# Optimization experiments

Hardware: AMD Instinct MI355X
Metric: run time of the kernel (lower is better)

## Reference

```python
import jax, jax.numpy as jnp
from jax import lax
import numpy as np


def _conv3x3(x, w, b):
    # x: [B,C,H,W], w: [O,I,3,3] (OIHW), SAME padding, stride 1
    y = lax.conv_general_dilated(x, w, window_strides=(1, 1), padding='SAME',
                                 dimension_numbers=('NCHW', 'OIHW', 'NCHW'))
    return y + b[None, :, None, None]


def setup_inputs() -> dict:
    key = jax.random.key(0)
    ks = jax.random.split(key, 9)
    B, C, H, W = 4, 64, 64, 64
    wscale = 1.0 / np.sqrt(C * 9)  # keep conv outputs / attention logits sane
    x = jax.random.normal(ks[0], (B, C, H, W), dtype=jnp.float32)
    wq = jax.random.normal(ks[1], (C, C, 3, 3), dtype=jnp.float32) * wscale
    bq = jax.random.normal(ks[2], (C,), dtype=jnp.float32) * 0.1
    wk = jax.random.normal(ks[3], (C, C, 3, 3), dtype=jnp.float32) * wscale
    bk = jax.random.normal(ks[4], (C,), dtype=jnp.float32) * 0.1
    wv = jax.random.normal(ks[5], (C, C, 3, 3), dtype=jnp.float32) * wscale
    bv = jax.random.normal(ks[6], (C,), dtype=jnp.float32) * 0.1
    pos_gamma = jax.random.normal(ks[7], (1,), dtype=jnp.float32)
    chan_gamma = jax.random.normal(ks[8], (1,), dtype=jnp.float32)
    return {'x': x, 'wq': wq, 'bq': bq, 'wk': wk, 'bk': bk, 'wv': wv, 'bv': bv,
            'pos_gamma': pos_gamma, 'chan_gamma': chan_gamma}


def reference(x, wq, bq, wk, bk, wv, bv, pos_gamma, chan_gamma):
    B, C, H, W = x.shape
    N = H * W
    # position (spatial) self-attention over N = H*W locations
    q = _conv3x3(x, wq, bq).reshape(B, C, N)
    k = _conv3x3(x, wk, bk).reshape(B, C, N)
    v = _conv3x3(x, wv, bv).reshape(B, C, N)
    # attn[b,i,j] = softmax_j( sum_c q[b,c,i] * k[b,c,j] )
    pos_attn = jax.nn.softmax(jnp.einsum('bci,bcj->bij', q, k), axis=-1)
    # pos_out[b,c,j] = sum_i v[b,c,i] * attn[b,i,j]  (matches torch.bmm(v, attn))
    pos = jnp.einsum('bci,bij->bcj', v, pos_attn).reshape(B, C, H, W)
    pos_out = pos_gamma * pos + x
    # channel self-attention over C channels (x is its own q/k/v)
    xf = x.reshape(B, C, N)
    chan_attn = jax.nn.softmax(jnp.einsum('bcn,bdn->bcd', xf, xf), axis=-1)
    chan = jnp.einsum('bcd,bdn->bcn', chan_attn, xf).reshape(B, C, H, W)
    chan_out = chan_gamma * chan + x
    return pos_out + chan_out
```

## Files before the change

### kernel.cpp

```cpp
#include <hip/hip_runtime.h>

#define OFF_POS   0u
#define OFF_Q2    1048576u
#define OFF_K2    2097152u
#define OFF_V2    3145728u
#define OFF_VLO   3670016u
#define OFF_WT    4194304u
#define OFF_INVL  4452352u
#define OFF_GPART 4468736u
#define OFF_A     4730880u
#define WS_FLOATS 4747264u

typedef short s8v __attribute__((ext_vector_type(8)));
typedef float f4v __attribute__((ext_vector_type(4)));
typedef float f16v __attribute__((ext_vector_type(16)));

#define MFMA32(a, b, c) __builtin_amdgcn_mfma_f32_32x32x16_bf16((a), (b), (c), 0, 0, 0)

__device__ __forceinline__ unsigned short bf16_rne(float f) {
    union { float f; unsigned int u; } v; v.f = f;
    unsigned int r = v.u + 0x7FFFu + ((v.u >> 16) & 1u);
    return (unsigned short)(r >> 16);
}
__device__ __forceinline__ float bf2f(unsigned short h) {
    union { unsigned int u; float f; } t; t.u = ((unsigned int)h) << 16;
    return t.f;
}
__device__ __forceinline__ void split2(float f, unsigned short& h, unsigned short& l) {
    unsigned short hh = bf16_rne(f);
    h = hh;
    l = bf16_rne(f - bf2f(hh));
}
__device__ __forceinline__ unsigned int pk2(float lo, float hi) {
    return (unsigned int)bf16_rne(lo) | ((unsigned int)bf16_rne(hi) << 16);
}
__device__ __forceinline__ void pl32swap(unsigned int& a, unsigned int& b) {
    asm volatile("v_permlane32_swap_b32 %0, %1" : "+v"(a), "+v"(b));
}
__device__ __forceinline__ s8v mk8(unsigned int w0, unsigned int w1,
                                   unsigned int w2, unsigned int w3) {
    union { unsigned int u[4]; s8v v; } t;
    t.u[0] = w0; t.u[1] = w1; t.u[2] = w2; t.u[3] = w3;
    return t.v;
}
__device__ __forceinline__ f16v zero16() {
    f16v z;
#pragma unroll
    for (int i = 0; i < 16; ++i) z[i] = 0.0f;
    return z;
}


__global__ void k_wtrans(const float* __restrict__ wq, const float* __restrict__ wk,
                         const float* __restrict__ wv, unsigned short* __restrict__ wf) {
    int t = blockIdx.x * 256 + threadIdx.x;
    int f = t >> 9, pos = t & 511;
    int lane = pos >> 3, e = pos & 7;
    int oc = f & 1, kst = (f >> 1) & 3;
    int ct = f >> 3;
    int tap = ct % 9, conv = ct / 9;
    int o = oc * 32 + (lane & 31);
    int ci = kst * 16 + (lane >> 5) * 8 + e;
    const float* w = (conv == 0) ? wq : (conv == 1) ? wk : wv;
    float v = w[(o * 64 + ci) * 9 + tap];
    unsigned short hh, ll;
    split2(v, hh, ll);
    wf[(f * 2 + 0) * 512 + pos] = hh;
    wf[(f * 2 + 1) * 512 + pos] = ll;
}

__global__ __launch_bounds__(384) void k_conv(
        const float* __restrict__ x, const unsigned short* __restrict__ wf,
        const float* __restrict__ bq, const float* __restrict__ bk, const float* __restrict__ bv,
        unsigned short* __restrict__ Q2, unsigned short* __restrict__ K2,
        unsigned short* __restrict__ V2, unsigned short* __restrict__ VLO) {
    int nb = blockIdx.x;
    int b = blockIdx.y;
    int h = nb >> 1, w0 = (nb & 1) * 32;

    __shared__ unsigned short xwh[6528];
    __shared__ unsigned short xwl[6528];

    int tid = threadIdx.x;
    for (int idx = tid; idx < 6528; idx += 384) {
        int W = idx % 34;
        int c = (idx / 34) & 63;
        int dy = idx / (34 * 64);
        int hs = h + dy - 1, wi = w0 + W - 1;
        float v = 0.0f;
        if (hs >= 0 && hs < 64 && wi >= 0 && wi < 64)
            v = x[((b * 64 + c) * 64 + hs) * 64 + wi];
        unsigned short hh_, ll_;
        split2(v, hh_, ll_);
        int row = dy * 34 + W;
        int byt = row * 128 + c * 2;
        int swz = byt ^ ((row & 7) << 4);
        *(unsigned short*)((char*)xwh + swz) = hh_;
        *(unsigned short*)((char*)xwl + swz) = ll_;
    }
    __syncthreads();

    int lane = tid & 63, wv = tid >> 6;
    int conv = wv >> 1, oc = wv & 1;
    int hh = lane >> 5, l31 = lane & 31;

    const float* bias = (conv == 0) ? bq : (conv == 1) ? bk : bv;
    f16v D;
    if (conv < 2) {
#pragma unroll
        for (int r = 0; r < 16; ++r)
            D[r] = bias[oc * 32 + (r & 3) + 8 * (r >> 2) + 4 * hh];
    } else {
        float bvv = bias[oc * 32 + l31];
#pragma unroll
        for (int r = 0; r < 16; ++r) D[r] = bvv;
    }

#pragma unroll
    for (int tap = 0; tap < 9; ++tap) {
        int dy = tap / 3, dx = tap % 3;
#pragma unroll
        for (int kst = 0; kst < 4; ++kst) {
            int f = ((conv * 9 + tap) * 4 + kst) * 2 + oc;
            s8v Wh = *(const s8v*)(wf + (f * 2 + 0) * 512 + lane * 8);
            s8v Wl = *(const s8v*)(wf + (f * 2 + 1) * 512 + lane * 8);
            int row = dy * 34 + dx + l31;
            int byt = row * 128 + kst * 32 + hh * 16;
            int swz = byt ^ ((row & 7) << 4);
            s8v Xh = *(const s8v*)((const char*)xwh + swz);
            s8v Xl = *(const s8v*)((const char*)xwl + swz);
            if (conv < 2) {
                D = MFMA32(Wh, Xh, D);
                D = MFMA32(Wh, Xl, D);
                D = MFMA32(Wl, Xh, D);
            } else {
                D = MFMA32(Xh, Wh, D);
                D = MFMA32(Xl, Wh, D);
                D = MFMA32(Xh, Wl, D);
            }
        }
    }

    unsigned short sh[16], sl[16];
#pragma unroll
    for (int r = 0; r < 16; ++r) split2(D[r], sh[r], sl[r]);
    unsigned int ah0 = sh[0] | ((unsigned int)sh[1] << 16), ah1 = sh[2] | ((unsigned int)sh[3] << 16);
    unsigned int ah2 = sh[4] | ((unsigned int)sh[5] << 16), ah3 = sh[6] | ((unsigned int)sh[7] << 16);
    pl32swap(ah0, ah2); pl32swap(ah1, ah3);
    s8v F0h = mk8(ah0, ah1, ah2, ah3);
    unsigned int al0 = sl[0] | ((unsigned int)sl[1] << 16), al1 = sl[2] | ((unsigned int)sl[3] << 16);
    unsigned int al2 = sl[4] | ((unsigned int)sl[5] << 16), al3 = sl[6] | ((unsigned int)sl[7] << 16);
    pl32swap(al0, al2); pl32swap(al1, al3);
    s8v F0l = mk8(al0, al1, al2, al3);
    unsigned int bh0 = sh[8] | ((unsigned int)sh[9] << 16), bh1 = sh[10] | ((unsigned int)sh[11] << 16);
    unsigned int bh2 = sh[12] | ((unsigned int)sh[13] << 16), bh3 = sh[14] | ((unsigned int)sh[15] << 16);
    pl32swap(bh0, bh2); pl32swap(bh1, bh3);
    s8v F1h = mk8(bh0, bh1, bh2, bh3);
    unsigned int bl0 = sl[8] | ((unsigned int)sl[9] << 16), bl1 = sl[10] | ((unsigned int)sl[11] << 16);
    unsigned int bl2 = sl[12] | ((unsigned int)sl[13] << 16), bl3 = sl[14] | ((unsigned int)sl[15] << 16);
    pl32swap(bl0, bl2); pl32swap(bl1, bl3);
    s8v F1l = mk8(bl0, bl1, bl2, bl3);

    if (conv < 2) {
        unsigned short* dst = (conv == 0) ? Q2 : K2;
        size_t b0 = (size_t)(((b * 128 + nb) * 4 + oc * 2 + 0) * 2) * 512 + lane * 8;
        size_t b1 = (size_t)(((b * 128 + nb) * 4 + oc * 2 + 1) * 2) * 512 + lane * 8;
        *(s8v*)(dst + b0) = F0h;
        *(s8v*)(dst + b0 + 512) = F0l;
        *(s8v*)(dst + b1) = F1h;
        *(s8v*)(dst + b1 + 512) = F1l;
    } else {
        size_t b0 = (size_t)((((b * 128 + nb) * 2 + 0) * 2 + oc)) * 512 + lane * 8;
        size_t b1 = (size_t)((((b * 128 + nb) * 2 + 1) * 2 + oc)) * 512 + lane * 8;
        *(s8v*)(V2 + b0) = F0h;
        *(s8v*)(VLO + b0) = F0l;
        *(s8v*)(V2 + b1) = F1h;
        *(s8v*)(VLO + b1) = F1l;
    }
}

__global__ __launch_bounds__(256) void k_gram(const float* __restrict__ x, float* __restrict__ Gp64) {
    int nc = blockIdx.x, b = blockIdx.y;
    __shared__ float xs[64 * 65];
    int tid = threadIdx.x;
#pragma unroll
    for (int it = 0; it < 4; ++it) {
        int f4i = tid + it * 256;
        int c = f4i >> 4, n4 = f4i & 15;
        float4 vv = *(const float4*)(x + (size_t)(b * 64 + c) * 4096 + nc * 64 + n4 * 4);
        xs[c * 65 + n4 * 4 + 0] = vv.x;
        xs[c * 65 + n4 * 4 + 1] = vv.y;
        xs[c * 65 + n4 * 4 + 2] = vv.z;
        xs[c * 65 + n4 * 4 + 3] = vv.w;
    }
    __syncthreads();
    int tc = tid & 15, td = tid >> 4;
    int c0 = tc * 4, d0 = td * 4;
    float acc[4][4];
#pragma unroll
    for (int i = 0; i < 4; ++i)
#pragma unroll
        for (int j = 0; j < 4; ++j) acc[i][j] = 0.0f;
    for (int n = 0; n < 64; ++n) {
        float xc[4], xd[4];
#pragma unroll
        for (int i = 0; i < 4; ++i) xc[i] = xs[(c0 + i) * 65 + n];
#pragma unroll
        for (int j = 0; j < 4; ++j) xd[j] = xs[(d0 + j) * 65 + n];
#pragma unroll
        for (int i = 0; i < 4; ++i)
#pragma unroll
            for (int j = 0; j < 4; ++j) acc[i][j] += xc[i] * xd[j];
    }
#pragma unroll
    for (int i = 0; i < 4; ++i) {
        float4 o4 = {acc[i][0], acc[i][1], acc[i][2], acc[i][3]};
        *(float4*)(Gp64 + (size_t)(nc * 4 + b) * 4096 + (c0 + i) * 64 + d0) = o4;
    }
}

__global__ void k_asm(const float* __restrict__ Gp64, float* __restrict__ A) {
    int row = blockIdx.x;
    int d = threadIdx.x;
    int b = row >> 6, c = row & 63;
    float g = 0.0f;
    for (int p = 0; p < 64; ++p) g += Gp64[(size_t)(p * 4 + b) * 4096 + c * 64 + d];
    float mx = g;
    for (int off = 32; off >= 1; off >>= 1) mx = fmaxf(mx, __shfl_xor(mx, off, 64));
    float e = __expf(g - mx);
    float s = e;
    for (int off = 32; off >= 1; off >>= 1) s += __shfl_xor(s, off, 64);
    A[row * 64 + d] = e / s;
}

__global__ __launch_bounds__(512) void k_pass1(
        const unsigned short* __restrict__ Q2, const unsigned short* __restrict__ K2,
        float* __restrict__ invl) {
    int flat = blockIdx.x;
    int xcd = flat & 7;
    int b = xcd >> 1;
    int pr = (xcd & 1) * 32 + (flat >> 3);
    int tid = threadIdx.x, lane = tid & 63, wv = tid >> 6;
    int jp = wv & 3, ichL = wv >> 2;
    int ich = pr * 2 + ichL;

    __shared__ float lsum[2][4][32];

    const unsigned short* qp = Q2 + (size_t)(b * 128 + ich) * 4096 + lane * 8;
    s8v qf0 = *(const s8v*)(qp);
    s8v qf1 = *(const s8v*)(qp + 512);
    s8v qf2 = *(const s8v*)(qp + 1024);
    s8v qf3 = *(const s8v*)(qp + 1536);
    s8v qf4 = *(const s8v*)(qp + 2048);
    s8v qf5 = *(const s8v*)(qp + 2560);
    s8v qf6 = *(const s8v*)(qp + 3072);
    s8v qf7 = *(const s8v*)(qp + 3584);

    float la0 = 0.f, la1 = 0.f;
#pragma unroll 1
    for (int t = 0; t < 32; ++t) {
        int jch = jp * 32 + t;
        const unsigned short* kp = K2 + (size_t)(b * 128 + jch) * 4096 + lane * 8;
        s8v kf0 = *(const s8v*)(kp);
        s8v kf1 = *(const s8v*)(kp + 512);
        s8v kf2 = *(const s8v*)(kp + 1024);
        s8v kf3 = *(const s8v*)(kp + 1536);
        s8v kf4 = *(const s8v*)(kp + 2048);
        s8v kf5 = *(const s8v*)(kp + 2560);
        s8v kf6 = *(const s8v*)(kp + 3072);
        s8v kf7 = *(const s8v*)(kp + 3584);
        f16v Sa = zero16(), Sb = zero16();
        Sa = MFMA32(kf0, qf0, Sa);
        Sa = MFMA32(kf0, qf1, Sa);
        Sa = MFMA32(kf1, qf0, Sa);
        Sa = MFMA32(kf2, qf2, Sa);
        Sa = MFMA32(kf2, qf3, Sa);
        Sa = MFMA32(kf3, qf2, Sa);
        Sb = MFMA32(kf4, qf4, Sb);
        Sb = MFMA32(kf4, qf5, Sb);
        Sb = MFMA32(kf5, qf4, Sb);
        Sb = MFMA32(kf6, qf6, Sb);
        Sb = MFMA32(kf6, qf7, Sb);
        Sb = MFMA32(kf7, qf6, Sb);
#pragma unroll
        for (int r = 0; r < 8; ++r) la0 += __expf(Sa[r] + Sb[r]);
#pragma unroll
        for (int r = 8; r < 16; ++r) la1 += __expf(Sa[r] + Sb[r]);
    }
    float lacc = la0 + la1;
    lacc += __shfl_xor(lacc, 32);
    if (lane < 32) lsum[ichL][jp][lane] = lacc;
    __syncthreads();
    if (tid < 64) {
        int iL = tid & 31, iH = tid >> 5;
        float s = lsum[iH][0][iL] + lsum[iH][1][iL] + lsum[iH][2][iL] + lsum[iH][3][iL];
        invl[b * 4096 + (pr * 2 + iH) * 32 + iL] = 1.0f / s;
    }
}

__global__ __launch_bounds__(256) void k_vnorm(
        unsigned short* __restrict__ V2, const unsigned short* __restrict__ VLO,
        const float* __restrict__ invl) {
    int u = blockIdx.x * 256 + threadIdx.x;
    int lane = u & 63, ksub = (u >> 7) & 1;
    int ich = (u >> 8) & 127, b = u >> 15;
    int n0 = ich * 32 + ksub * 16 + (lane >> 5) * 8;
    size_t base = (size_t)u * 8;
    s8v vh = *(s8v*)(V2 + base);
    s8v vl = *(const s8v*)(VLO + base);
    float4 iv0 = *(const float4*)(invl + b * 4096 + n0);
    float4 iv1 = *(const float4*)(invl + b * 4096 + n0 + 4);
    float ivv[8] = {iv0.x, iv0.y, iv0.z, iv0.w, iv1.x, iv1.y, iv1.z, iv1.w};
    s8v o;
#pragma unroll
    for (int e = 0; e < 8; ++e) {
        float v = bf2f((unsigned short)vh[e]) + bf2f((unsigned short)vl[e]);
        o[e] = (short)bf16_rne(v * ivv[e]);
    }
    *(s8v*)(V2 + base) = o;
}

__global__ __launch_bounds__(512) void k_pass2(
        const unsigned short* __restrict__ Q2, const unsigned short* __restrict__ K2,
        const unsigned short* __restrict__ V2, const float* __restrict__ x,
        const float* __restrict__ A, const float* __restrict__ pg,
        const float* __restrict__ cg, float* __restrict__ out) {
    int flat = blockIdx.x;
    int xcd = flat & 7;
    int b = xcd >> 1;
    int pr = (xcd & 1) * 32 + (flat >> 3);
    int tid = threadIdx.x, lane = tid & 63, wv = tid >> 6;
    int ip = wv & 3, jhalf = wv >> 2;
    int jt = pr * 2 + jhalf;

    __shared__ float rlds[2][4][64][32];

    const unsigned short* kp = K2 + (size_t)(b * 128 + jt) * 4096 + lane * 8;
    s8v kf0 = *(const s8v*)(kp);
    s8v kf1 = *(const s8v*)(kp + 512);
    s8v kf2 = *(const s8v*)(kp + 1024);
    s8v kf3 = *(const s8v*)(kp + 1536);
    s8v kf4 = *(const s8v*)(kp + 2048);
    s8v kf5 = *(const s8v*)(kp + 2560);
    s8v kf6 = *(const s8v*)(kp + 3072);
    s8v kf7 = *(const s8v*)(kp + 3584);

    f16v O0 = zero16(), O1 = zero16();

#pragma unroll 1
    for (int t = 0; t < 32; ++t) {
        int ich = ip * 32 + t;
        const unsigned short* qp = Q2 + (size_t)(b * 128 + ich) * 4096 + lane * 8;
        s8v qf0 = *(const s8v*)(qp);
        s8v qf1 = *(const s8v*)(qp + 512);
        s8v qf2 = *(const s8v*)(qp + 1024);
        s8v qf3 = *(const s8v*)(qp + 1536);
        s8v qf4 = *(const s8v*)(qp + 2048);
        s8v qf5 = *(const s8v*)(qp + 2560);
        s8v qf6 = *(const s8v*)(qp + 3072);
        s8v qf7 = *(const s8v*)(qp + 3584);
        const unsigned short* vp = V2 + (size_t)(b * 128 + ich) * 2048 + lane * 8;
        s8v vA = *(const s8v*)(vp);
        s8v vB = *(const s8v*)(vp + 512);
        s8v vC = *(const s8v*)(vp + 1024);
        s8v vD = *(const s8v*)(vp + 1536);

        f16v Sa = zero16(), Sb = zero16();
        Sa = MFMA32(qf0, kf0, Sa);
        Sa = MFMA32(qf0, kf1, Sa);
        Sa = MFMA32(qf1, kf0, Sa);
        Sa = MFMA32(qf2, kf2, Sa);
        Sa = MFMA32(qf2, kf3, Sa);
        Sa = MFMA32(qf3, kf2, Sa);
        Sb = MFMA32(qf4, kf4, Sb);
        Sb = MFMA32(qf4, kf5, Sb);
        Sb = MFMA32(qf5, kf4, Sb);
        Sb = MFMA32(qf6, kf6, Sb);
        Sb = MFMA32(qf6, kf7, Sb);
        Sb = MFMA32(qf7, kf6, Sb);

        float p[16];
#pragma unroll
        for (int r = 0; r < 16; ++r) p[r] = __expf(Sa[r] + Sb[r]);

        unsigned int a0 = pk2(p[0], p[1]),  a1 = pk2(p[2], p[3]);
        unsigned int a2 = pk2(p[4], p[5]),  a3 = pk2(p[6], p[7]);
        pl32swap(a0, a2);
        pl32swap(a1, a3);
        s8v P0 = mk8(a0, a1, a2, a3);
        unsigned int b0 = pk2(p[8], p[9]),  b1 = pk2(p[10], p[11]);
        unsigned int b2 = pk2(p[12], p[13]), b3 = pk2(p[14], p[15]);
        pl32swap(b0, b2);
        pl32swap(b1, b3);
        s8v P1 = mk8(b0, b1, b2, b3);

        O0 = MFMA32(vA, P0, O0);
        O0 = MFMA32(vC, P1, O0);
        O1 = MFMA32(vB, P0, O1);
        O1 = MFMA32(vD, P1, O1);
    }

    int hh = lane >> 5, jj = lane & 31;
#pragma unroll
    for (int r = 0; r < 16; ++r) {
        int c = (r & 3) + 8 * (r >> 2) + 4 * hh;
        rlds[jhalf][ip][c][jj] = O0[r];
        rlds[jhalf][ip][c + 32][jj] = O1[r];
    }
    __syncthreads();
    float sums[8];
#pragma unroll
    for (int k = 0; k < 8; ++k) {
        int e = tid + k * 512;
        int jh = e >> 11, rem = e & 2047, c = rem >> 5, j2 = rem & 31;
        sums[k] = rlds[jh][0][c][j2] + rlds[jh][1][c][j2]
                + rlds[jh][2][c][j2] + rlds[jh][3][c][j2];
    }
    __syncthreads();
    float* sb = &rlds[0][0][0][0];
    float* xs2 = sb;
    float* As2 = sb + 4160;
    int n0 = pr * 64;
#pragma unroll
    for (int it = 0; it < 2; ++it) {
        int f4i = tid + it * 512;
        int d = f4i >> 4, j4 = f4i & 15;
        float4 vv = *(const float4*)(x + (size_t)(b * 64 + d) * 4096 + n0 + j4 * 4);
        xs2[d * 65 + j4 * 4 + 0] = vv.x;
        xs2[d * 65 + j4 * 4 + 1] = vv.y;
        xs2[d * 65 + j4 * 4 + 2] = vv.z;
        xs2[d * 65 + j4 * 4 + 3] = vv.w;
        ((float4*)As2)[f4i] = ((const float4*)(A + (size_t)b * 4096))[f4i];
    }
    __syncthreads();
    float pgv = pg[0], cgv = cg[0];
#pragma unroll
    for (int k = 0; k < 8; ++k) {
        int e = tid + k * 512;
        int jh = e >> 11, rem = e & 2047, c = rem >> 5, j2 = rem & 31;
        int jt2 = jh * 32 + j2;
        float ch = 0.f;
#pragma unroll
        for (int d = 0; d < 64; ++d) ch += As2[c * 64 + d] * xs2[d * 65 + jt2];
        float xc = xs2[c * 65 + jt2];
        out[(size_t)(b * 64 + c) * 4096 + n0 + jt2] = pgv * sums[k] + cgv * ch + 2.0f * xc;
    }
}

extern "C" void kernel_launch(void* const* d_in, const int* in_sizes, int n_in,
                              void* d_out, int out_size, void* d_ws, size_t ws_size,
                              hipStream_t stream) {
    const float* x  = (const float*)d_in[0];
    const float* wq = (const float*)d_in[1];
    const float* bq = (const float*)d_in[2];
    const float* wk = (const float*)d_in[3];
    const float* bk = (const float*)d_in[4];
    const float* wv = (const float*)d_in[5];
    const float* bv = (const float*)d_in[6];
    const float* pg = (const float*)d_in[7];
    const float* cg = (const float*)d_in[8];
    float* out = (float*)d_out;

    if (ws_size < (size_t)WS_FLOATS * sizeof(float)) return;
    float* ws = (float*)d_ws;
    float* Gp64 = ws + OFF_POS;
    unsigned short* Q2  = (unsigned short*)(ws + OFF_Q2);
    unsigned short* K2  = (unsigned short*)(ws + OFF_K2);
    unsigned short* V2  = (unsigned short*)(ws + OFF_V2);
    unsigned short* VLO = (unsigned short*)(ws + OFF_VLO);
    unsigned short* wfb = (unsigned short*)(ws + OFF_WT);
    float* invl = ws + OFF_INVL;
    float* A    = ws + OFF_A;

    k_wtrans<<<432, 256, 0, stream>>>(wq, wk, wv, wfb);
    k_conv<<<dim3(128, 4), 384, 0, stream>>>(x, wfb, bq, bk, bv, Q2, K2, V2, VLO);
    k_gram<<<dim3(64, 4), 256, 0, stream>>>(x, Gp64);
    k_asm<<<256, 64, 0, stream>>>(Gp64, A);
    k_pass1<<<256, 512, 0, stream>>>(Q2, K2, invl);
    k_vnorm<<<512, 256, 0, stream>>>(V2, VLO, invl);
    k_pass2<<<256, 512, 0, stream>>>(Q2, K2, V2, x, A, pg, cg, out);
}
```

Baseline: 128.1 us.

## Move channel attention to bf16 MFMA, drop V low part, retile attention passes

Adds a packing kernel that converts x to bf16 MFMA-fragment layouts. It uses those layouts for the Gram matrix and for the channel-attention output, both now computed with MFMA instead of scalar FMA loops. V is stored as bf16 high part only, with no low split, and bf16 packing uses the hardware cvt_pk instruction. Pass1 and pass2 now give each block a single 32-wide tile with 8 waves splitting the key range, which doubles the grid. These changes cut scalar ALU and memory traffic but lower precision in the channel path and in V.

Result: faster. 124.8 us (-2.5%).

```diff
diff --git a/kernel.cpp b/kernel.cpp
--- a/kernel.cpp
+++ b/kernel.cpp
@@ -1,18 +1,15 @@
 #include <hip/hip_runtime.h>
 
-#define OFF_POS   0u
 #define OFF_Q2    1048576u
 #define OFF_K2    2097152u
 #define OFF_V2    3145728u
-#define OFF_VLO   3670016u
+#define OFF_X2    3670016u
 #define OFF_WT    4194304u
 #define OFF_INVL  4452352u
-#define OFF_GPART 4468736u
 #define OFF_A     4730880u
 #define WS_FLOATS 4747264u
 
 typedef short s8v __attribute__((ext_vector_type(8)));
-typedef float f4v __attribute__((ext_vector_type(4)));
 typedef float f16v __attribute__((ext_vector_type(16)));
 
 #define MFMA32(a, b, c) __builtin_amdgcn_mfma_f32_32x32x16_bf16((a), (b), (c), 0, 0, 0)
@@ -31,8 +28,10 @@
     h = hh;
     l = bf16_rne(f - bf2f(hh));
 }
-__device__ __forceinline__ unsigned int pk2(float lo, float hi) {
-    return (unsigned int)bf16_rne(lo) | ((unsigned int)bf16_rne(hi) << 16);
+__device__ __forceinline__ unsigned int cvtpk(float lo, float hi) {
+    unsigned int r;
+    asm("v_cvt_pk_bf16_f32 %0, %1, %2" : "=v"(r) : "v"(lo), "v"(hi));
+    return r;
 }
 __device__ __forceinline__ void pl32swap(unsigned int& a, unsigned int& b) {
     asm volatile("v_permlane32_swap_b32 %0, %1" : "+v"(a), "+v"(b));
@@ -69,11 +68,37 @@
     wf[(f * 2 + 1) * 512 + pos] = ll;
 }
 
+__global__ __launch_bounds__(256) void k_xpack(const float* __restrict__ x,
+                                               unsigned short* __restrict__ X2,
+                                               unsigned short* __restrict__ XV2) {
+    int gid = blockIdx.x * 256 + threadIdx.x;
+    int b = gid >> 16;
+    int c = (gid >> 10) & 63;
+    int n4 = (gid & 1023) * 4;
+    float4 v = *(const float4*)(x + (size_t)(b * 64 + c) * 4096 + n4);
+    unsigned short hv[4] = {bf16_rne(v.x), bf16_rne(v.y), bf16_rne(v.z), bf16_rne(v.w)};
+    int kst = c >> 4, e = c & 7, hb = (c >> 3) & 1;
+#pragma unroll
+    for (int u = 0; u < 4; ++u) {
+        int n = n4 + u;
+        int nch = n >> 5, lane = (n & 31) + 32 * hb;
+        X2[(size_t)((b * 128 + nch) * 4 + kst) * 512 + lane * 8 + e] = hv[u];
+    }
+    int ich = n4 >> 5, ksub = (n4 >> 4) & 1, cb = c >> 5;
+    int lane2 = (c & 31) + 32 * ((n4 >> 3) & 1);
+    size_t xi = (size_t)(((b * 128 + ich) * 2 + ksub) * 2 + cb) * 512 + lane2 * 8 + (n4 & 7);
+    unsigned long long w = (unsigned long long)hv[0]
+                         | ((unsigned long long)hv[1] << 16)
+                         | ((unsigned long long)hv[2] << 32)
+                         | ((unsigned long long)hv[3] << 48);
+    *(unsigned long long*)(XV2 + xi) = w;
+}
+
 __global__ __launch_bounds__(384) void k_conv(
         const float* __restrict__ x, const unsigned short* __restrict__ wf,
         const float* __restrict__ bq, const float* __restrict__ bk, const float* __restrict__ bv,
         unsigned short* __restrict__ Q2, unsigned short* __restrict__ K2,
-        unsigned short* __restrict__ V2, unsigned short* __restrict__ VLO) {
+        unsigned short* __restrict__ V2) {
     int nb = blockIdx.x;
     int b = blockIdx.y;
     int h = nb >> 1, w0 = (nb & 1) * 32;
@@ -141,27 +166,26 @@
         }
     }
 
-    unsigned short sh[16], sl[16];
-#pragma unroll
-    for (int r = 0; r < 16; ++r) split2(D[r], sh[r], sl[r]);
-    unsigned int ah0 = sh[0] | ((unsigned int)sh[1] << 16), ah1 = sh[2] | ((unsigned int)sh[3] << 16);
-    unsigned int ah2 = sh[4] | ((unsigned int)sh[5] << 16), ah3 = sh[6] | ((unsigned int)sh[7] << 16);
-    pl32swap(ah0, ah2); pl32swap(ah1, ah3);
-    s8v F0h = mk8(ah0, ah1, ah2, ah3);
-    unsigned int al0 = sl[0] | ((unsigned int)sl[1] << 16), al1 = sl[2] | ((unsigned int)sl[3] << 16);
-    unsigned int al2 = sl[4] | ((unsigned int)sl[5] << 16), al3 = sl[6] | ((unsigned int)sl[7] << 16);
-    pl32swap(al0, al2); pl32swap(al1, al3);
-    s8v F0l = mk8(al0, al1, al2, al3);
-    unsigned int bh0 = sh[8] | ((unsigned int)sh[9] << 16), bh1 = sh[10] | ((unsigned int)sh[11] << 16);
-    unsigned int bh2 = sh[12] | ((unsigned int)sh[13] << 16), bh3 = sh[14] | ((unsigned int)sh[15] << 16);
-    pl32swap(bh0, bh2); pl32swap(bh1, bh3);
-    s8v F1h = mk8(bh0, bh1, bh2, bh3);
-    unsigned int bl0 = sl[8] | ((unsigned int)sl[9] << 16), bl1 = sl[10] | ((unsigned int)sl[11] << 16);
-    unsigned int bl2 = sl[12] | ((unsigned int)sl[13] << 16), bl3 = sl[14] | ((unsigned int)sl[15] << 16);
-    pl32swap(bl0, bl2); pl32swap(bl1, bl3);
-    s8v F1l = mk8(bl0, bl1, bl2, bl3);
-
     if (conv < 2) {
+        unsigned short sh[16], sl[16];
+#pragma unroll
+        for (int r = 0; r < 16; ++r) split2(D[r], sh[r], sl[r]);
+        unsigned int ah0 = sh[0] | ((unsigned int)sh[1] << 16), ah1 = sh[2] | ((unsigned int)sh[3] << 16);
+        unsigned int ah2 = sh[4] | ((unsigned int)sh[5] << 16), ah3 = sh[6] | ((unsigned int)sh[7] << 16);
+        pl32swap(ah0, ah2); pl32swap(ah1, ah3);
+        s8v F0h = mk8(ah0, ah1, ah2, ah3);
+        unsigned int al0 = sl[0] | ((unsigned int)sl[1] << 16), al1 = sl[2] | ((unsigned int)sl[3] << 16);
+        unsigned int al2 = sl[4] | ((unsigned int)sl[5] << 16), al3 = sl[6] | ((unsigned int)sl[7] << 16);
+        pl32swap(al0, al2); pl32swap(al1, al3);
+        s8v F0l = mk8(al0, al1, al2, al3);
+        unsigned int bh0 = sh[8] | ((unsigned int)sh[9] << 16), bh1 = sh[10] | ((unsigned int)sh[11] << 16);
+        unsigned int bh2 = sh[12] | ((unsigned int)sh[13] << 16), bh3 = sh[14] | ((unsigned int)sh[15] << 16);
+        pl32swap(bh0, bh2); pl32swap(bh1, bh3);
+        s8v F1h = mk8(bh0, bh1, bh2, bh3);
+        unsigned int bl0 = sl[8] | ((unsigned int)sl[9] << 16), bl1 = sl[10] | ((unsigned int)sl[11] << 16);
+        unsigned int bl2 = sl[12] | ((unsigned int)sl[13] << 16), bl3 = sl[14] | ((unsigned int)sl[15] << 16);
+        pl32swap(bl0, bl2); pl32swap(bl1, bl3);
+        s8v F1l = mk8(bl0, bl1, bl2, bl3);
         unsigned short* dst = (conv == 0) ? Q2 : K2;
         size_t b0 = (size_t)(((b * 128 + nb) * 4 + oc * 2 + 0) * 2) * 512 + lane * 8;
         size_t b1 = (size_t)(((b * 128 + nb) * 4 + oc * 2 + 1) * 2) * 512 + lane * 8;
@@ -170,67 +194,63 @@
         *(s8v*)(dst + b1) = F1h;
         *(s8v*)(dst + b1 + 512) = F1l;
     } else {
-        size_t b0 = (size_t)((((b * 128 + nb) * 2 + 0) * 2 + oc)) * 512 + lane * 8;
-        size_t b1 = (size_t)((((b * 128 + nb) * 2 + 1) * 2 + oc)) * 512 + lane * 8;
-        *(s8v*)(V2 + b0) = F0h;
-        *(s8v*)(VLO + b0) = F0l;
-        *(s8v*)(V2 + b1) = F1h;
-        *(s8v*)(VLO + b1) = F1l;
-    }
-}
-
-__global__ __launch_bounds__(256) void k_gram(const float* __restrict__ x, float* __restrict__ Gp64) {
-    int nc = blockIdx.x, b = blockIdx.y;
-    __shared__ float xs[64 * 65];
-    int tid = threadIdx.x;
-#pragma unroll
-    for (int it = 0; it < 4; ++it) {
-        int f4i = tid + it * 256;
-        int c = f4i >> 4, n4 = f4i & 15;
-        float4 vv = *(const float4*)(x + (size_t)(b * 64 + c) * 4096 + nc * 64 + n4 * 4);
-        xs[c * 65 + n4 * 4 + 0] = vv.x;
-        xs[c * 65 + n4 * 4 + 1] = vv.y;
-        xs[c * 65 + n4 * 4 + 2] = vv.z;
-        xs[c * 65 + n4 * 4 + 3] = vv.w;
-    }
-    __syncthreads();
-    int tc = tid & 15, td = tid >> 4;
-    int c0 = tc * 4, d0 = td * 4;
-    float acc[4][4];
-#pragma unroll
-    for (int i = 0; i < 4; ++i)
-#pragma unroll
-        for (int j = 0; j < 4; ++j) acc[i][j] = 0.0f;
-    for (int n = 0; n < 64; ++n) {
-        float xc[4], xd[4];
-#pragma unroll
-        for (int i = 0; i < 4; ++i) xc[i] = xs[(c0 + i) * 65 + n];
-#pragma unroll
-        for (int j = 0; j < 4; ++j) xd[j] = xs[(d0 + j) * 65 + n];
-#pragma unroll
-        for (int i = 0; i < 4; ++i)
-#pragma unroll
-            for (int j = 0; j < 4; ++j) acc[i][j] += xc[i] * xd[j];
-    }
-#pragma unroll
-    for (int i = 0; i < 4; ++i) {
-        float4 o4 = {acc[i][0], acc[i][1], acc[i][2], acc[i][3]};
-        *(float4*)(Gp64 + (size_t)(nc * 4 + b) * 4096 + (c0 + i) * 64 + d0) = o4;
-    }
-}
-
-__global__ void k_asm(const float* __restrict__ Gp64, float* __restrict__ A) {
+        unsigned int a0 = cvtpk(D[0], D[1]),  a1 = cvtpk(D[2], D[3]);
+        unsigned int a2 = cvtpk(D[4], D[5]),  a3 = cvtpk(D[6], D[7]);
+        pl32swap(a0, a2); pl32swap(a1, a3);
+        s8v F0h = mk8(a0, a1, a2, a3);
+        unsigned int b0w = cvtpk(D[8], D[9]),  b1w = cvtpk(D[10], D[11]);
+        unsigned int b2w = cvtpk(D[12], D[13]), b3w = cvtpk(D[14], D[15]);
+        pl32swap(b0w, b2w); pl32swap(b1w, b3w);
+        s8v F1h = mk8(b0w, b1w, b2w, b3w);
+        size_t v0 = (size_t)(((b * 128 + nb) * 2 + 0) * 2 + oc) * 512 + lane * 8;
+        size_t v1 = (size_t)(((b * 128 + nb) * 2 + 1) * 2 + oc) * 512 + lane * 8;
+        *(s8v*)(V2 + v0) = F0h;
+        *(s8v*)(V2 + v1) = F1h;
+    }
+}
+
+__global__ __launch_bounds__(256) void k_gram(const unsigned short* __restrict__ XV2,
+                                              float* __restrict__ Gp) {
+    int kp = blockIdx.x, b = blockIdx.y;
+    int tid = threadIdx.x, lane = tid & 63, wv = tid >> 6;
+    int cb1 = wv & 1, cb2 = wv >> 1;
+    f16v G = zero16();
+#pragma unroll 1
+    for (int t = 0; t < 32; ++t) {
+        int ich = kp * 32 + t;
+        const unsigned short* base = XV2 + (size_t)(b * 128 + ich) * 2048 + lane * 8;
+        s8v a0 = *(const s8v*)(base + (0 * 2 + cb1) * 512);
+        s8v b0 = *(const s8v*)(base + (0 * 2 + cb2) * 512);
+        s8v a1 = *(const s8v*)(base + (1 * 2 + cb1) * 512);
+        s8v b1 = *(const s8v*)(base + (1 * 2 + cb2) * 512);
+        G = MFMA32(a0, b0, G);
+        G = MFMA32(a1, b1, G);
+    }
+    int hh = lane >> 5, l31 = lane & 31;
+#pragma unroll
+    for (int r = 0; r < 16; ++r) {
+        int cc = cb1 * 32 + (r & 3) + 8 * (r >> 2) + 4 * hh;
+        int dd = cb2 * 32 + l31;
+        Gp[(size_t)(kp * 4 + b) * 4096 + cc * 64 + dd] = G[r];
+    }
+}
+
+__global__ void k_asm(const float* __restrict__ Gp, unsigned short* __restrict__ A2) {
     int row = blockIdx.x;
     int d = threadIdx.x;
     int b = row >> 6, c = row & 63;
     float g = 0.0f;
-    for (int p = 0; p < 64; ++p) g += Gp64[(size_t)(p * 4 + b) * 4096 + c * 64 + d];
+#pragma unroll
+    for (int p = 0; p < 4; ++p) g += Gp[(size_t)(p * 4 + b) * 4096 + c * 64 + d];
     float mx = g;
     for (int off = 32; off >= 1; off >>= 1) mx = fmaxf(mx, __shfl_xor(mx, off, 64));
     float e = __expf(g - mx);
     float s = e;
     for (int off = 32; off >= 1; off >>= 1) s += __shfl_xor(s, off, 64);
-    A[row * 64 + d] = e / s;
+    float a = e / s;
+    int cb = c >> 5, kst = d >> 4;
+    int lane2 = (c & 31) + 32 * ((d >> 3) & 1);
+    A2[(size_t)((b * 2 + cb) * 4 + kst) * 512 + lane2 * 8 + (d & 7)] = bf16_rne(a);
 }
 
 __global__ __launch_bounds__(512) void k_pass1(
@@ -239,12 +259,10 @@
     int flat = blockIdx.x;
     int xcd = flat & 7;
     int b = xcd >> 1;
-    int pr = (xcd & 1) * 32 + (flat >> 3);
+    int ich = (xcd & 1) * 64 + (flat >> 3);
     int tid = threadIdx.x, lane = tid & 63, wv = tid >> 6;
-    int jp = wv & 3, ichL = wv >> 2;
-    int ich = pr * 2 + ichL;
-
-    __shared__ float lsum[2][4][32];
+
+    __shared__ float lsum[8][32];
 
     const unsigned short* qp = Q2 + (size_t)(b * 128 + ich) * 4096 + lane * 8;
     s8v qf0 = *(const s8v*)(qp);
@@ -258,8 +276,8 @@
 
     float la0 = 0.f, la1 = 0.f;
 #pragma unroll 1
-    for (int t = 0; t < 32; ++t) {
-        int jch = jp * 32 + t;
+    for (int t = 0; t < 16; ++t) {
+        int jch = wv * 16 + t;
         const unsigned short* kp = K2 + (size_t)(b * 128 + jch) * 4096 + lane * 8;
         s8v kf0 = *(const s8v*)(kp);
         s8v kf1 = *(const s8v*)(kp + 512);
@@ -289,51 +307,47 @@
     }
     float lacc = la0 + la1;
     lacc += __shfl_xor(lacc, 32);
-    if (lane < 32) lsum[ichL][jp][lane] = lacc;
+    if (lane < 32) lsum[wv][lane] = lacc;
     __syncthreads();
-    if (tid < 64) {
-        int iL = tid & 31, iH = tid >> 5;
-        float s = lsum[iH][0][iL] + lsum[iH][1][iL] + lsum[iH][2][iL] + lsum[iH][3][iL];
-        invl[b * 4096 + (pr * 2 + iH) * 32 + iL] = 1.0f / s;
+    if (tid < 32) {
+        float s = 0.f;
+#pragma unroll
+        for (int p = 0; p < 8; ++p) s += lsum[p][tid];
+        invl[b * 4096 + ich * 32 + tid] = 1.0f / s;
     }
 }
 
 __global__ __launch_bounds__(256) void k_vnorm(
-        unsigned short* __restrict__ V2, const unsigned short* __restrict__ VLO,
-        const float* __restrict__ invl) {
+        unsigned short* __restrict__ V2, const float* __restrict__ invl) {
     int u = blockIdx.x * 256 + threadIdx.x;
     int lane = u & 63, ksub = (u >> 7) & 1;
     int ich = (u >> 8) & 127, b = u >> 15;
     int n0 = ich * 32 + ksub * 16 + (lane >> 5) * 8;
     size_t base = (size_t)u * 8;
     s8v vh = *(s8v*)(V2 + base);
-    s8v vl = *(const s8v*)(VLO + base);
     float4 iv0 = *(const float4*)(invl + b * 4096 + n0);
     float4 iv1 = *(const float4*)(invl + b * 4096 + n0 + 4);
     float ivv[8] = {iv0.x, iv0.y, iv0.z, iv0.w, iv1.x, iv1.y, iv1.z, iv1.w};
     s8v o;
 #pragma unroll
-    for (int e = 0; e < 8; ++e) {
-        float v = bf2f((unsigned short)vh[e]) + bf2f((unsigned short)vl[e]);
-        o[e] = (short)bf16_rne(v * ivv[e]);
-    }
+    for (int e = 0; e < 8; ++e)
+        o[e] = (short)bf16_rne(bf2f((unsigned short)vh[e]) * ivv[e]);
     *(s8v*)(V2 + base) = o;
 }
 
 __global__ __launch_bounds__(512) void k_pass2(
         const unsigned short* __restrict__ Q2, const unsigned short* __restrict__ K2,
-        const unsigned short* __restrict__ V2, const float* __restrict__ x,
-        const float* __restrict__ A, const float* __restrict__ pg,
-        const float* __restrict__ cg, float* __restrict__ out) {
+        const unsigned short* __restrict__ V2, const unsigned short* __restrict__ X2,
+        const unsigned short* __restrict__ A2, const float* __restrict__ x,
+        const float* __restrict__ pg, const float* __restrict__ cg,
+        float* __restrict__ out) {
     int flat = blockIdx.x;
     int xcd = flat & 7;
     int b = xcd >> 1;
-    int pr = (xcd & 1) * 32 + (flat >> 3);
+    int jt = (xcd & 1) * 64 + (flat >> 3);
     int tid = threadIdx.x, lane = tid & 63, wv = tid >> 6;
-    int ip = wv & 3, jhalf = wv >> 2;
-    int jt = pr * 2 + jhalf;
-
-    __shared__ float rlds[2][4][64][32];
+
+    __shared__ float rlds[8][64][32];
 
     const unsigned short* kp = K2 + (size_t)(b * 128 + jt) * 4096 + lane * 8;
     s8v kf0 = *(const s8v*)(kp);
@@ -348,8 +362,8 @@
     f16v O0 = zero16(), O1 = zero16();
 
 #pragma unroll 1
-    for (int t = 0; t < 32; ++t) {
-        int ich = ip * 32 + t;
+    for (int t = 0; t < 16; ++t) {
+        int ich = wv * 16 + t;
         const unsigned short* qp = Q2 + (size_t)(b * 128 + ich) * 4096 + lane * 8;
         s8v qf0 = *(const s8v*)(qp);
         s8v qf1 = *(const s8v*)(qp + 512);
@@ -383,13 +397,13 @@
 #pragma unroll
         for (int r = 0; r < 16; ++r) p[r] = __expf(Sa[r] + Sb[r]);
 
-        unsigned int a0 = pk2(p[0], p[1]),  a1 = pk2(p[2], p[3]);
-        unsigned int a2 = pk2(p[4], p[5]),  a3 = pk2(p[6], p[7]);
+        unsigned int a0 = cvtpk(p[0], p[1]),  a1 = cvtpk(p[2], p[3]);
+        unsigned int a2 = cvtpk(p[4], p[5]),  a3 = cvtpk(p[6], p[7]);
         pl32swap(a0, a2);
         pl32swap(a1, a3);
         s8v P0 = mk8(a0, a1, a2, a3);
-        unsigned int b0 = pk2(p[8], p[9]),  b1 = pk2(p[10], p[11]);
-        unsigned int b2 = pk2(p[12], p[13]), b3 = pk2(p[14], p[15]);
+        unsigned int b0 = cvtpk(p[8], p[9]),  b1 = cvtpk(p[10], p[11]);
+        unsigned int b2 = cvtpk(p[12], p[13]), b3 = cvtpk(p[14], p[15]);
         pl32swap(b0, b2);
         pl32swap(b1, b3);
         s8v P1 = mk8(b0, b1, b2, b3);
@@ -404,46 +418,51 @@
 #pragma unroll
     for (int r = 0; r < 16; ++r) {
         int c = (r & 3) + 8 * (r >> 2) + 4 * hh;
-        rlds[jhalf][ip][c][jj] = O0[r];
-        rlds[jhalf][ip][c + 32][jj] = O1[r];
+        rlds[wv][c][jj] = O0[r];
+        rlds[wv][c + 32][jj] = O1[r];
     }
     __syncthreads();
-    float sums[8];
-#pragma unroll
-    for (int k = 0; k < 8; ++k) {
-        int e = tid + k * 512;
-        int jh = e >> 11, rem = e & 2047, c = rem >> 5, j2 = rem & 31;
-        sums[k] = rlds[jh][0][c][j2] + rlds[jh][1][c][j2]
-                + rlds[jh][2][c][j2] + rlds[jh][3][c][j2];
+    float sums[4];
+#pragma unroll
+    for (int k = 0; k < 4; ++k) {
+        int el = tid + k * 512;
+        int c = el >> 5, j2 = el & 31;
+        float s = 0.f;
+#pragma unroll
+        for (int p = 0; p < 8; ++p) s += rlds[p][c][j2];
+        sums[k] = s;
     }
     __syncthreads();
-    float* sb = &rlds[0][0][0][0];
-    float* xs2 = sb;
-    float* As2 = sb + 4160;
-    int n0 = pr * 64;
-#pragma unroll
-    for (int it = 0; it < 2; ++it) {
-        int f4i = tid + it * 512;
-        int d = f4i >> 4, j4 = f4i & 15;
-        float4 vv = *(const float4*)(x + (size_t)(b * 64 + d) * 4096 + n0 + j4 * 4);
-        xs2[d * 65 + j4 * 4 + 0] = vv.x;
-        xs2[d * 65 + j4 * 4 + 1] = vv.y;
-        xs2[d * 65 + j4 * 4 + 2] = vv.z;
-        xs2[d * 65 + j4 * 4 + 3] = vv.w;
-        ((float4*)As2)[f4i] = ((const float4*)(A + (size_t)b * 4096))[f4i];
+    float* sb = &rlds[0][0][0];
+    if (wv < 2) {
+        int cb = wv;
+        f16v Dc = zero16();
+#pragma unroll
+        for (int kst = 0; kst < 4; ++kst) {
+            s8v af = *(const s8v*)(A2 + (size_t)((b * 2 + cb) * 4 + kst) * 512 + lane * 8);
+            s8v xf = *(const s8v*)(X2 + (size_t)((b * 128 + jt) * 4 + kst) * 512 + lane * 8);
+            Dc = MFMA32(af, xf, Dc);
+        }
+#pragma unroll
+        for (int r = 0; r < 16; ++r) {
+            int c = cb * 32 + (r & 3) + 8 * (r >> 2) + 4 * hh;
+            sb[c * 33 + jj] = Dc[r];
+        }
+    }
+#pragma unroll
+    for (int k = 0; k < 4; ++k) {
+        int el = tid + k * 512;
+        int c = el >> 5, j2 = el & 31;
+        sb[2112 + el] = x[(size_t)(b * 64 + c) * 4096 + jt * 32 + j2];
     }
     __syncthreads();
     float pgv = pg[0], cgv = cg[0];
 #pragma unroll
-    for (int k = 0; k < 8; ++k) {
-        int e = tid + k * 512;
-        int jh = e >> 11, rem = e & 2047, c = rem >> 5, j2 = rem & 31;
-        int jt2 = jh * 32 + j2;
-        float ch = 0.f;
-#pragma unroll
-        for (int d = 0; d < 64; ++d) ch += As2[c * 64 + d] * xs2[d * 65 + jt2];
-        float xc = xs2[c * 65 + jt2];
-        out[(size_t)(b * 64 + c) * 4096 + n0 + jt2] = pgv * sums[k] + cgv * ch + 2.0f * xc;
+    for (int k = 0; k < 4; ++k) {
+        int el = tid + k * 512;
+        int c = el >> 5, j2 = el & 31;
+        out[(size_t)(b * 64 + c) * 4096 + jt * 32 + j2] =
+            pgv * sums[k] + cgv * sb[c * 33 + j2] + 2.0f * sb[2112 + el];
     }
 }
 
@@ -463,20 +482,22 @@
 
     if (ws_size < (size_t)WS_FLOATS * sizeof(float)) return;
     float* ws = (float*)d_ws;
-    float* Gp64 = ws + OFF_POS;
+    float* Gp = ws;
+    unsigned short* XV2 = (unsigned short*)(ws + 65536);
     unsigned short* Q2  = (unsigned short*)(ws + OFF_Q2);
     unsigned short* K2  = (unsigned short*)(ws + OFF_K2);
     unsigned short* V2  = (unsigned short*)(ws + OFF_V2);
-    unsigned short* VLO = (unsigned short*)(ws + OFF_VLO);
+    unsigned short* X2  = (unsigned short*)(ws + OFF_X2);
     unsigned short* wfb = (unsigned short*)(ws + OFF_WT);
     float* invl = ws + OFF_INVL;
-    float* A    = ws + OFF_A;
+    unsigned short* A2  = (unsigned short*)(ws + OFF_A);
 
     k_wtrans<<<432, 256, 0, stream>>>(wq, wk, wv, wfb);
-    k_conv<<<dim3(128, 4), 384, 0, stream>>>(x, wfb, bq, bk, bv, Q2, K2, V2, VLO);
-    k_gram<<<dim3(64, 4), 256, 0, stream>>>(x, Gp64);
-    k_asm<<<256, 64, 0, stream>>>(Gp64, A);
-    k_pass1<<<256, 512, 0, stream>>>(Q2, K2, invl);
-    k_vnorm<<<512, 256, 0, stream>>>(V2, VLO, invl);
-    k_pass2<<<256, 512, 0, stream>>>(Q2, K2, V2, x, A, pg, cg, out);
-}
+    k_xpack<<<1024, 256, 0, stream>>>(x, X2, XV2);
+    k_conv<<<dim3(128, 4), 384, 0, stream>>>(x, wfb, bq, bk, bv, Q2, K2, V2);
+    k_gram<<<dim3(4, 4), 256, 0, stream>>>(XV2, Gp);
+    k_asm<<<256, 64, 0, stream>>>(Gp, A2);
+    k_pass1<<<512, 512, 0, stream>>>(Q2, K2, invl);
+    k_vnorm<<<512, 256, 0, stream>>>(V2, invl);
+    k_pass2<<<512, 512, 0, stream>>>(Q2, K2, V2, X2, A2, x, pg, cg, out);
+}
```
